# Kernel tuning notes

Measured on AMD Instinct MI355X. Metric: run time of the kernel, lower is better.

The kernel has to match this reference:

```python
import jax, jax.numpy as jnp
import numpy as np

EPS = 1e-6

def _sobel_kernels():
    kx = np.array([[1, 0, -1], [2, 0, -2], [1, 0, -1]], dtype=np.float32)
    ky = np.array([[1, 2, 1], [0, 0, 0], [-1, -2, -1]], dtype=np.float32)
    # [out=2, in=1, 3, 3]
    return jnp.asarray(np.stack([kx, ky])[:, None, :, :])

def _edge_mag(img):
    # img: [B, 3, H, W] -> per-channel sobel gradient magnitude [B, 3, H-2, W-2]
    B, C, H, W = img.shape
    x = img.reshape(B * C, 1, H, W)
    g = jax.lax.conv_general_dilated(
        x, _sobel_kernels(), window_strides=(1, 1), padding='VALID',
        dimension_numbers=('NCHW', 'OIHW', 'NCHW'))  # [B*C, 2, H-2, W-2]
    gx, gy = g[:, 0], g[:, 1]
    mag = jnp.sqrt(gx * gx + gy * gy)
    return mag.reshape(B, C, H - 2, W - 2)

def setup_inputs() -> dict:
    key = jax.random.key(0)
    k1, k2 = jax.random.split(key)
    shape = (16, 3, 512, 512)
    source = jax.random.uniform(k1, shape, dtype=jnp.float32)
    target = jax.random.uniform(k2, shape, dtype=jnp.float32)
    return {"source": source, "target": target}

def reference(source, target):
    edge_x = _edge_mag(source)
    edge_y = _edge_mag(target)
    diff = edge_x - edge_y
    error = jnp.sqrt(diff * diff + EPS)
    return jnp.sum(error) / source.shape[0]
```

## Files before the change

kernel.cpp:

```cpp
#include <hip/hip_runtime.h>

#define IMG_W 512
#define IMG_H 512
#define OUT_W 510
#define OUT_H 510
#define NPLANE 48
#define RPW 3
#define WPB 4
#define RPB 6
#define SPP (OUT_H / RPB)
#define NB (NPLANE * SPP)
#define NXCD 8
#define CPX (NB / NXCD)
#define NWIN (RPW + 2)
#define EPS 1e-6f

template <bool ATOMIC>
__global__ __launch_bounds__(256) void sobel_partial_kernel(
    const float* __restrict__ src, const float* __restrict__ tgt,
    float* __restrict__ partial)
{
    const int tid  = threadIdx.x;
    const int lane = tid & 63;
    const int wv   = tid >> 6;
    const int half = wv & 1;
    const int rg   = wv >> 1;
    const int xb   = half * 256 + lane * 4;

    const int b  = (blockIdx.x % NXCD) * CPX + blockIdx.x / NXCD;
    const int p  = b / SPP;
    const int y0 = (b - p * SPP) * RPB + rg * RPW;

    const size_t pb = (size_t)p * IMG_W * IMG_H + (size_t)y0 * IMG_W;
    const float* ps = src + pb + xb;
    const float* pt = tgt + pb + xb;
    const int seamoff = half ? 254 : 256;
    const float* ss = src + pb + seamoff;
    const float* st = tgt + pb + seamoff;

    float  vS[NWIN][4], vT[NWIN][4];
    float2 smS[NWIN], smT[NWIN];

    auto loadS = [&](int r) {
        float4 a = *reinterpret_cast<const float4*>(ps + (size_t)r * IMG_W);
        vS[r][0] = a.x; vS[r][1] = a.y; vS[r][2] = a.z; vS[r][3] = a.w;
    };
    auto loadT = [&](int r) {
        float4 a = *reinterpret_cast<const float4*>(pt + (size_t)r * IMG_W);
        vT[r][0] = a.x; vT[r][1] = a.y; vT[r][2] = a.z; vT[r][3] = a.w;
    };

    loadS(0); loadS(1); loadS(2);
    loadT(0); loadT(1); loadT(2);
    #pragma unroll
    for (int r = 0; r < NWIN; ++r) {
        smS[r] = *reinterpret_cast<const float2*>(ss + (size_t)r * IMG_W);
        smT[r] = *reinterpret_cast<const float2*>(st + (size_t)r * IMG_W);
    }
    loadS(3); loadT(3);
    loadS(4); loadT(4);

    const bool l63 = (lane == 63);
    float e0S[NWIN], e1S[NWIN], e0T[NWIN], e1T[NWIN];
    auto halo = [&](int r) {
        float a = __shfl_down(vS[r][0], 1, 64);
        float b2 = __shfl_down(vS[r][1], 1, 64);
        float c = __shfl_down(vT[r][0], 1, 64);
        float d = __shfl_down(vT[r][1], 1, 64);
        e0S[r] = l63 ? smS[r].x : a;
        e1S[r] = l63 ? smS[r].y : b2;
        e0T[r] = l63 ? smT[r].x : c;
        e1T[r] = l63 ? smT[r].y : d;
    };

    auto VS = [&](int r, int k) -> float {
        return k < 4 ? vS[r][k] : (k == 4 ? e0S[r] : e1S[r]);
    };
    auto VT = [&](int r, int k) -> float {
        return k < 4 ? vT[r][k] : (k == 4 ? e0T[r] : e1T[r]);
    };

    float cm[4];
    #pragma unroll
    for (int j = 0; j < 4; ++j) cm[j] = (xb + j < OUT_W) ? 1.0f : 0.0f;

    float acc = 0.0f;

    #pragma unroll
    for (int i = 0; i < RPW; ++i) {
        if (i == 0) { halo(0); halo(1); halo(2); }
        else        { halo(i + 2); }

        const int a = i, bb = i + 1, c = i + 2;
        float rowsum = 0.0f;

        #pragma unroll
        for (int j = 0; j < 4; ++j) {
            float gxs = fmaf(2.0f, VS(bb, j) - VS(bb, j + 2),
                             (VS(a, j) - VS(a, j + 2)) + (VS(c, j) - VS(c, j + 2)));
            float gys = fmaf(2.0f, VS(a, j + 1), VS(a, j) + VS(a, j + 2))
                      - fmaf(2.0f, VS(c, j + 1), VS(c, j) + VS(c, j + 2));
            float ms  = __builtin_amdgcn_sqrtf(fmaf(gxs, gxs, gys * gys));

            float gxt = fmaf(2.0f, VT(bb, j) - VT(bb, j + 2),
                             (VT(a, j) - VT(a, j + 2)) + (VT(c, j) - VT(c, j + 2)));
            float gyt = fmaf(2.0f, VT(a, j + 1), VT(a, j) + VT(a, j + 2))
                      - fmaf(2.0f, VT(c, j + 1), VT(c, j) + VT(c, j + 2));
            float mt  = __builtin_amdgcn_sqrtf(fmaf(gxt, gxt, gyt * gyt));

            float e = fabsf(ms - mt);
            rowsum = fmaf(e, cm[j], rowsum);
        }

        acc += rowsum;
    }

    #pragma unroll
    for (int off = 32; off > 0; off >>= 1)
        acc += __shfl_down(acc, off, 64);

    __shared__ float wsum[WPB];
    if (lane == 0) wsum[wv] = acc;
    __syncthreads();
    if (tid == 0) {
        float tot = wsum[0] + wsum[1] + wsum[2] + wsum[3];
        if (ATOMIC) atomicAdd(partial, tot * (1.0f / 16.0f));
        else        partial[blockIdx.x] = tot;
    }
}

__global__ __launch_bounds__(1024) void reduce_kernel(
    const float* __restrict__ partial, float* __restrict__ out)
{
    float acc = 0.0f;
    for (int i = threadIdx.x; i < NB; i += 1024) acc += partial[i];

    #pragma unroll
    for (int off = 32; off > 0; off >>= 1)
        acc += __shfl_down(acc, off, 64);

    __shared__ float wsum[16];
    const int lane = threadIdx.x & 63;
    const int wid  = threadIdx.x >> 6;
    if (lane == 0) wsum[wid] = acc;
    __syncthreads();
    if (wid == 0) {
        float v = (lane < 16) ? wsum[lane] : 0.0f;
        #pragma unroll
        for (int off = 8; off > 0; off >>= 1)
            v += __shfl_down(v, off, 64);
        if (lane == 0) out[0] = v * (1.0f / 16.0f);
    }
}

extern "C" void kernel_launch(void* const* d_in, const int* in_sizes, int n_in,
                              void* d_out, int out_size, void* d_ws, size_t ws_size,
                              hipStream_t stream) {
    const float* src = (const float*)d_in[0];
    const float* tgt = (const float*)d_in[1];
    float* out = (float*)d_out;

    if (ws_size >= (size_t)NB * sizeof(float)) {
        float* partial = (float*)d_ws;
        sobel_partial_kernel<false><<<dim3(NB), dim3(256), 0, stream>>>(src, tgt, partial);
        reduce_kernel<<<dim3(1), dim3(1024), 0, stream>>>(partial, out);
    } else {
        hipMemsetAsync(out, 0, (size_t)out_size * sizeof(float), stream);
        sobel_partial_kernel<true><<<dim3(NB), dim3(256), 0, stream>>>(src, tgt, out);
    }
}
```

Measured before the change: 22.99 us.

## Process two strips per block and load halo directly instead of shuffles

```diff
diff --git a/kernel.cpp b/kernel.cpp
--- a/kernel.cpp
+++ b/kernel.cpp
@@ -9,11 +9,14 @@
 #define WPB 4
 #define RPB 6
 #define SPP (OUT_H / RPB)
-#define NB (NPLANE * SPP)
+#define NSTRIP (NPLANE * SPP)
+#define NB (NSTRIP / 2)
 #define NXCD 8
 #define CPX (NB / NXCD)
 #define NWIN (RPW + 2)
 #define EPS 1e-6f
+
+struct RowW { float v[6]; };
 
 template <bool ATOMIC>
 __global__ __launch_bounds__(256) void sobel_partial_kernel(
@@ -26,94 +29,79 @@
     const int half = wv & 1;
     const int rg   = wv >> 1;
     const int xb   = half * 256 + lane * 4;
+    const int o2   = (half == 1 && lane == 63) ? -2 : 4;
 
     const int b  = (blockIdx.x % NXCD) * CPX + blockIdx.x / NXCD;
-    const int p  = b / SPP;
-    const int y0 = (b - p * SPP) * RPB + rg * RPW;
+    const int sA = 2 * b, sB = 2 * b + 1;
 
-    const size_t pb = (size_t)p * IMG_W * IMG_H + (size_t)y0 * IMG_W;
-    const float* ps = src + pb + xb;
-    const float* pt = tgt + pb + xb;
-    const int seamoff = half ? 254 : 256;
-    const float* ss = src + pb + seamoff;
-    const float* st = tgt + pb + seamoff;
+    const int pA = sA / SPP, pB = sB / SPP;
+    const int yA = (sA - pA * SPP) * RPB + rg * RPW;
+    const int yB = (sB - pB * SPP) * RPB + rg * RPW;
 
-    float  vS[NWIN][4], vT[NWIN][4];
-    float2 smS[NWIN], smT[NWIN];
+    const float* psA = src + (size_t)pA * IMG_W * IMG_H + (size_t)yA * IMG_W + xb;
+    const float* ptA = tgt + (size_t)pA * IMG_W * IMG_H + (size_t)yA * IMG_W + xb;
+    const float* psB = src + (size_t)pB * IMG_W * IMG_H + (size_t)yB * IMG_W + xb;
+    const float* ptB = tgt + (size_t)pB * IMG_W * IMG_H + (size_t)yB * IMG_W + xb;
 
-    auto loadS = [&](int r) {
-        float4 a = *reinterpret_cast<const float4*>(ps + (size_t)r * IMG_W);
-        vS[r][0] = a.x; vS[r][1] = a.y; vS[r][2] = a.z; vS[r][3] = a.w;
-    };
-    auto loadT = [&](int r) {
-        float4 a = *reinterpret_cast<const float4*>(pt + (size_t)r * IMG_W);
-        vT[r][0] = a.x; vT[r][1] = a.y; vT[r][2] = a.z; vT[r][3] = a.w;
-    };
-
-    loadS(0); loadS(1); loadS(2);
-    loadT(0); loadT(1); loadT(2);
-    #pragma unroll
-    for (int r = 0; r < NWIN; ++r) {
-        smS[r] = *reinterpret_cast<const float2*>(ss + (size_t)r * IMG_W);
-        smT[r] = *reinterpret_cast<const float2*>(st + (size_t)r * IMG_W);
-    }
-    loadS(3); loadT(3);
-    loadS(4); loadT(4);
-
-    const bool l63 = (lane == 63);
-    float e0S[NWIN], e1S[NWIN], e0T[NWIN], e1T[NWIN];
-    auto halo = [&](int r) {
-        float a = __shfl_down(vS[r][0], 1, 64);
-        float b2 = __shfl_down(vS[r][1], 1, 64);
-        float c = __shfl_down(vT[r][0], 1, 64);
-        float d = __shfl_down(vT[r][1], 1, 64);
-        e0S[r] = l63 ? smS[r].x : a;
-        e1S[r] = l63 ? smS[r].y : b2;
-        e0T[r] = l63 ? smT[r].x : c;
-        e1T[r] = l63 ? smT[r].y : d;
-    };
-
-    auto VS = [&](int r, int k) -> float {
-        return k < 4 ? vS[r][k] : (k == 4 ? e0S[r] : e1S[r]);
-    };
-    auto VT = [&](int r, int k) -> float {
-        return k < 4 ? vT[r][k] : (k == 4 ? e0T[r] : e1T[r]);
+    auto loadRow = [&](const float* q, RowW& w) {
+        float4 a = *reinterpret_cast<const float4*>(q);
+        float2 c = *reinterpret_cast<const float2*>(q + o2);
+        w.v[0] = a.x; w.v[1] = a.y; w.v[2] = a.z; w.v[3] = a.w;
+        w.v[4] = c.x; w.v[5] = c.y;
     };
 
     float cm[4];
     #pragma unroll
     for (int j = 0; j < 4; ++j) cm[j] = (xb + j < OUT_W) ? 1.0f : 0.0f;
 
+    auto rowcalc = [&](const RowW& s0, const RowW& s1, const RowW& s2,
+                       const RowW& t0, const RowW& t1, const RowW& t2) -> float {
+        float rs = 0.0f;
+        #pragma unroll
+        for (int j = 0; j < 4; ++j) {
+            float gxs = fmaf(2.0f, s1.v[j] - s1.v[j + 2],
+                             (s0.v[j] - s0.v[j + 2]) + (s2.v[j] - s2.v[j + 2]));
+            float gys = fmaf(2.0f, s0.v[j + 1], s0.v[j] + s0.v[j + 2])
+                      - fmaf(2.0f, s2.v[j + 1], s2.v[j] + s2.v[j + 2]);
+            float ms  = __builtin_amdgcn_sqrtf(fmaf(gxs, gxs, gys * gys));
+
+            float gxt = fmaf(2.0f, t1.v[j] - t1.v[j + 2],
+                             (t0.v[j] - t0.v[j + 2]) + (t2.v[j] - t2.v[j + 2]));
+            float gyt = fmaf(2.0f, t0.v[j + 1], t0.v[j] + t0.v[j + 2])
+                      - fmaf(2.0f, t2.v[j + 1], t2.v[j] + t2.v[j + 2]);
+            float mt  = __builtin_amdgcn_sqrtf(fmaf(gxt, gxt, gyt * gyt));
+
+            rs = fmaf(fabsf(ms - mt), cm[j], rs);
+        }
+        return rs;
+    };
+
+    RowW aS[NWIN], aT[NWIN], bS[NWIN], bT[NWIN];
+
+    #pragma unroll
+    for (int r = 0; r < NWIN; ++r) {
+        loadRow(psA + (size_t)r * IMG_W, aS[r]);
+        loadRow(ptA + (size_t)r * IMG_W, aT[r]);
+    }
+    #pragma unroll
+    for (int r = 0; r < 3; ++r) {
+        loadRow(psB + (size_t)r * IMG_W, bS[r]);
+        loadRow(ptB + (size_t)r * IMG_W, bT[r]);
+    }
+
     float acc = 0.0f;
 
-    #pragma unroll
-    for (int i = 0; i < RPW; ++i) {
-        if (i == 0) { halo(0); halo(1); halo(2); }
-        else        { halo(i + 2); }
+    acc += rowcalc(aS[0], aS[1], aS[2], aT[0], aT[1], aT[2]);
+    loadRow(psB + (size_t)3 * IMG_W, bS[3]);
+    loadRow(ptB + (size_t)3 * IMG_W, bT[3]);
+    acc += rowcalc(aS[1], aS[2], aS[3], aT[1], aT[2], aT[3]);
+    loadRow(psB + (size_t)4 * IMG_W, bS[4]);
+    loadRow(ptB + (size_t)4 * IMG_W, bT[4]);
+    acc += rowcalc(aS[2], aS[3], aS[4], aT[2], aT[3], aT[4]);
 
-        const int a = i, bb = i + 1, c = i + 2;
-        float rowsum = 0.0f;
-
-        #pragma unroll
-        for (int j = 0; j < 4; ++j) {
-            float gxs = fmaf(2.0f, VS(bb, j) - VS(bb, j + 2),
-                             (VS(a, j) - VS(a, j + 2)) + (VS(c, j) - VS(c, j + 2)));
-            float gys = fmaf(2.0f, VS(a, j + 1), VS(a, j) + VS(a, j + 2))
-                      - fmaf(2.0f, VS(c, j + 1), VS(c, j) + VS(c, j + 2));
-            float ms  = __builtin_amdgcn_sqrtf(fmaf(gxs, gxs, gys * gys));
-
-            float gxt = fmaf(2.0f, VT(bb, j) - VT(bb, j + 2),
-                             (VT(a, j) - VT(a, j + 2)) + (VT(c, j) - VT(c, j + 2)));
-            float gyt = fmaf(2.0f, VT(a, j + 1), VT(a, j) + VT(a, j + 2))
-                      - fmaf(2.0f, VT(c, j + 1), VT(c, j) + VT(c, j + 2));
-            float mt  = __builtin_amdgcn_sqrtf(fmaf(gxt, gxt, gyt * gyt));
-
-            float e = fabsf(ms - mt);
-            rowsum = fmaf(e, cm[j], rowsum);
-        }
-
-        acc += rowsum;
-    }
+    acc += rowcalc(bS[0], bS[1], bS[2], bT[0], bT[1], bT[2]);
+    acc += rowcalc(bS[1], bS[2], bS[3], bT[1], bT[2], bT[3]);
+    acc += rowcalc(bS[2], bS[3], bS[4], bT[2], bT[3], bT[4]);
 
     #pragma unroll
     for (int off = 32; off > 0; off >>= 1)
```

New measurement: 24.85 us. 1.08x slower.
